# Optimization experiments

Measured on AMD Instinct MI355X. Metric: run time of the kernel, lower is better.

Reference implementation:

```python
import jax, jax.numpy as jnp
import numpy as np

N_NODES = 100000
N_EDGES = 1600000
NFEAT = 128
NHID = 128
NCLASS = 40


def setup_inputs() -> dict:
    key = jax.random.key(0)
    ks = jax.random.split(key, 12)
    s = 0.05
    return {
        "x": jax.random.normal(ks[0], (N_NODES, NFEAT), jnp.float32),
        "edge_index": jax.random.randint(ks[1], (2, N_EDGES), 0, N_NODES, jnp.int64),
        "W_pre": jax.random.normal(ks[2], (NHID, NFEAT), jnp.float32) * s,
        "b_pre": jax.random.normal(ks[3], (NHID,), jnp.float32) * s,
        "Wl0": jax.random.normal(ks[4], (NHID, NHID), jnp.float32) * s,
        "bl0": jax.random.normal(ks[5], (NHID,), jnp.float32) * s,
        "Wr0": jax.random.normal(ks[6], (NHID, NHID), jnp.float32) * s,
        "Wl1": jax.random.normal(ks[7], (NHID, NHID), jnp.float32) * s,
        "bl1": jax.random.normal(ks[8], (NHID,), jnp.float32) * s,
        "Wr1": jax.random.normal(ks[9], (NHID, NHID), jnp.float32) * s,
        "W_post": jax.random.normal(ks[10], (NCLASS, NHID), jnp.float32) * s,
        "b_post": jax.random.normal(ks[11], (NCLASS,), jnp.float32) * s,
    }


def _sage_conv(x, src, dst, Wl, bl, Wr):
    # PyG SAGEConv (mean aggr): out = lin_l(mean_{j->i} x_j) + lin_r(x_i)
    n = x.shape[0]
    agg = jax.ops.segment_sum(x[src], dst, num_segments=n)  # [N, H]
    cnt = jax.ops.segment_sum(jnp.ones((src.shape[0],), x.dtype), dst, num_segments=n)
    agg = agg / jnp.maximum(cnt, 1.0)[:, None]
    return agg @ Wl.T + bl + x @ Wr.T


def reference(x, edge_index, W_pre, b_pre, Wl0, bl0, Wr0, Wl1, bl1, Wr1, W_post, b_post):
    src, dst = edge_index[0], edge_index[1]
    h = x @ W_pre.T + b_pre  # pre-linear
    h = jax.nn.relu(_sage_conv(h, src, dst, Wl0, bl0, Wr0))  # dropout identity (eval)
    h = jax.nn.relu(_sage_conv(h, src, dst, Wl1, bl1, Wr1))
    logits = h @ W_post.T + b_post
    return jax.nn.log_softmax(logits, axis=1)
```

## Files before the change

kernel.cpp:

```cpp
#include <hip/hip_runtime.h>
#include <hip/hip_bf16.h>
#include <math.h>

#define N_NODES 100000
#define N_EDGES 1600000
#define NF 128
#define NC 40

#define NB 256
#define NPB 391
#define CAP 8192
#define PART_BLOCKS 512
#define PART_E ((N_EDGES + PART_BLOCKS - 1) / PART_BLOCKS)

#define WB_ELEMS (5 * 16384 + 48 * 128)

typedef __attribute__((ext_vector_type(8))) short short8v;
typedef __attribute__((ext_vector_type(4))) float f32x4;
typedef __attribute__((ext_vector_type(2))) float f32x2;
typedef unsigned short ushort_t;

__device__ inline float bflo(unsigned v) { union { unsigned u; float f; } x; x.u = v << 16; return x.f; }
__device__ inline float bfhi(unsigned v) { union { unsigned u; float f; } x; x.u = v & 0xffff0000u; return x.f; }
__device__ inline ushort_t f2bf(float f) {
    __hip_bfloat16 h = __float2bfloat16(f);
    return __builtin_bit_cast(ushort_t, h);
}

__device__ inline void acc_fp8x8p(uint2 v, f32x2& a0, f32x2& a1, f32x2& a2, f32x2& a3) {
    a0 += __builtin_amdgcn_cvt_pk_f32_fp8((int)v.x, false);
    a1 += __builtin_amdgcn_cvt_pk_f32_fp8((int)v.x, true);
    a2 += __builtin_amdgcn_cvt_pk_f32_fp8((int)v.y, false);
    a3 += __builtin_amdgcn_cvt_pk_f32_fp8((int)v.y, true);
}

__device__ inline short8v cvt_f32x8_bf16(float4 f0, float4 f1) {
    short8v v;
    v[0] = (short)f2bf(f0.x); v[1] = (short)f2bf(f0.y);
    v[2] = (short)f2bf(f0.z); v[3] = (short)f2bf(f0.w);
    v[4] = (short)f2bf(f1.x); v[5] = (short)f2bf(f1.y);
    v[6] = (short)f2bf(f1.z); v[7] = (short)f2bf(f1.w);
    return v;
}


__global__ __launch_bounds__(256) void k_part(const int* __restrict__ src,
                                              const int* __restrict__ dst,
                                              unsigned* __restrict__ bcur,
                                              uint2* __restrict__ pairs) {
    __shared__ unsigned cnt[NB];
    __shared__ unsigned curs[NB];
    const int t = threadIdx.x;
    cnt[t] = 0;
    __syncthreads();
    const int e0 = blockIdx.x * PART_E;
    int e1 = e0 + PART_E; if (e1 > N_EDGES) e1 = N_EDGES;
    for (int e = e0 + t; e < e1; e += 256)
        atomicAdd(&cnt[dst[e] / NPB], 1u);
    __syncthreads();
    unsigned c = cnt[t];
    curs[t] = c ? atomicAdd(&bcur[t], c) : 0u;
    __syncthreads();
    for (int e = e0 + t; e < e1; e += 256) {
        int d = dst[e];
        int s = src[e];
        int b = d / NPB;
        unsigned p = atomicAdd(&curs[b], 1u);
        if (p < CAP) pairs[(size_t)b * CAP + p] = make_uint2((unsigned)d, (unsigned)s);
    }
}

__global__ void k_bscan(const unsigned* __restrict__ bcur,
                        unsigned* __restrict__ bbase,
                        unsigned* __restrict__ rowptr) {
    __shared__ unsigned s[NB];
    const int t = threadIdx.x;
    unsigned v = bcur[t];
    s[t] = v; __syncthreads();
    for (int off = 1; off < NB; off <<= 1) {
        unsigned u = (t >= off) ? s[t - off] : 0;
        __syncthreads();
        s[t] += u;
        __syncthreads();
    }
    bbase[t] = s[t] - v;
    if (t == NB - 1) rowptr[N_NODES] = s[NB - 1];
}

__global__ __launch_bounds__(256) void k_bucket(const uint2* __restrict__ pairs,
                                                const unsigned* __restrict__ bcur,
                                                const unsigned* __restrict__ bbase,
                                                unsigned* __restrict__ rowptr,
                                                unsigned* __restrict__ srcs) {
    __shared__ unsigned s[512];
    const int t = threadIdx.x;
    const int b = blockIdx.x;
    unsigned cnt = bcur[b]; if (cnt > CAP) cnt = CAP;
    const unsigned base = bbase[b];
    const int n0 = b * NPB;
    int nn = N_NODES - n0; if (nn > NPB) nn = NPB;
    const uint2* pp = pairs + (size_t)b * CAP;

    s[t] = 0; s[t + 256] = 0;
    __syncthreads();
    for (unsigned i = t; i < cnt; i += 256)
        atomicAdd(&s[pp[i].x - n0], 1u);
    __syncthreads();
    unsigned d0 = s[t], d1 = s[t + 256];
    for (int off = 1; off < 512; off <<= 1) {
        unsigned u0 = (t >= off) ? s[t - off] : 0;
        unsigned u1 = (t + 256 >= off) ? s[t + 256 - off] : 0;
        __syncthreads();
        s[t] += u0; s[t + 256] += u1;
        __syncthreads();
    }
    unsigned ex0 = base + s[t] - d0;
    unsigned ex1 = base + s[t + 256] - d1;
    __syncthreads();
    s[t] = ex0; s[t + 256] = ex1;
    if (t < nn) rowptr[n0 + t] = ex0;
    if (t + 256 < nn) rowptr[n0 + t + 256] = ex1;
    __syncthreads();
    for (unsigned i = t; i < cnt; i += 256) {
        uint2 e = pp[i];
        unsigned p = atomicAdd(&s[e.x - n0], 1u);
        srcs[p] = e.y;
    }
}


__global__ void k_castw(const float* __restrict__ w0, const float* __restrict__ w1,
                        const float* __restrict__ w2, const float* __restrict__ w3,
                        const float* __restrict__ w4, const float* __restrict__ wp,
                        ushort_t* __restrict__ out) {
    int i = blockIdx.x * 256 + threadIdx.x;
    if (i < 5 * 16384) {
        int m = i >> 14, j = i & 16383;
        const float* s = (m == 0) ? w0 : (m == 1) ? w1 : (m == 2) ? w2 : (m == 3) ? w3 : w4;
        out[i] = f2bf(s[j]);
    } else if (i < WB_ELEMS) {
        int j = i - 5 * 16384;
        int row = j >> 7, col = j & 127;
        out[i] = (row < NC) ? f2bf(wp[row * NF + col]) : (ushort_t)0;
    }
}


__global__ __launch_bounds__(256) void k_aggregate8(const uint2* __restrict__ h64,
                                                    const unsigned* __restrict__ rowptr,
                                                    const unsigned* __restrict__ srcs,
                                                    ushort_t* __restrict__ agg) {
    int wave = threadIdx.x >> 6;
    int lane = threadIdx.x & 63;
    int node = blockIdx.x * 4 + wave;
    if (node >= N_NODES) return;
    const int slot = lane >> 4;
    const int d = lane & 15;
    unsigned beg = rowptr[node], end = rowptr[node + 1];
    f32x2 a0 = {0.f, 0.f}, a1 = {0.f, 0.f}, a2 = {0.f, 0.f}, a3 = {0.f, 0.f};
    unsigned i = beg;
    for (; i + 16 <= end; i += 16) {
        unsigned s0 = srcs[i + slot];
        unsigned s1 = srcs[i + 4 + slot];
        unsigned s2 = srcs[i + 8 + slot];
        unsigned s3 = srcs[i + 12 + slot];
        uint2 v0 = h64[(size_t)s0 * 16 + d];
        uint2 v1 = h64[(size_t)s1 * 16 + d];
        uint2 v2 = h64[(size_t)s2 * 16 + d];
        uint2 v3 = h64[(size_t)s3 * 16 + d];
        acc_fp8x8p(v0, a0, a1, a2, a3);
        acc_fp8x8p(v1, a0, a1, a2, a3);
        acc_fp8x8p(v2, a0, a1, a2, a3);
        acc_fp8x8p(v3, a0, a1, a2, a3);
    }
    if (i + 8 <= end) {
        unsigned s0 = srcs[i + slot];
        unsigned s1 = srcs[i + 4 + slot];
        uint2 v0 = h64[(size_t)s0 * 16 + d];
        uint2 v1 = h64[(size_t)s1 * 16 + d];
        acc_fp8x8p(v0, a0, a1, a2, a3);
        acc_fp8x8p(v1, a0, a1, a2, a3);
        i += 8;
    }
    if (i + 4 <= end) {
        unsigned s0 = srcs[i + slot];
        uint2 v0 = h64[(size_t)s0 * 16 + d];
        acc_fp8x8p(v0, a0, a1, a2, a3);
        i += 4;
    }
    if (i + slot < end) {
        unsigned s0 = srcs[i + slot];
        uint2 v0 = h64[(size_t)s0 * 16 + d];
        acc_fp8x8p(v0, a0, a1, a2, a3);
    }
    float r[8] = {a0.x, a0.y, a1.x, a1.y, a2.x, a2.y, a3.x, a3.y};
#pragma unroll
    for (int j = 0; j < 8; ++j) {
        r[j] += __shfl_xor(r[j], 16, 64);
        r[j] += __shfl_xor(r[j], 32, 64);
    }
    if (slot == 0) {
        float sc = 1.f / fmaxf((float)(end - beg), 1.f);
        uint4 o;
        o.x = ((unsigned)f2bf(r[1] * sc) << 16) | (unsigned)f2bf(r[0] * sc);
        o.y = ((unsigned)f2bf(r[3] * sc) << 16) | (unsigned)f2bf(r[2] * sc);
        o.z = ((unsigned)f2bf(r[5] * sc) << 16) | (unsigned)f2bf(r[4] * sc);
        o.w = ((unsigned)f2bf(r[7] * sc) << 16) | (unsigned)f2bf(r[6] * sc);
        ((uint4*)(agg + (size_t)node * NF))[d] = o;
    }
}


template <int SRC_F32, int HAS2>
__global__ __launch_bounds__(512, 4) void k_gemm2(const void* __restrict__ A1v,
                                                  const ushort_t* __restrict__ A2,
                                                  const ushort_t* __restrict__ W1,
                                                  const ushort_t* __restrict__ W2,
                                                  const float* __restrict__ bias,
                                                  ushort_t* __restrict__ out,
                                                  unsigned char* __restrict__ out8) {
    constexpr int WLDS = HAS2 ? 65536 : 32768;
    __shared__ char ldsc[WLDS + 16384];
    char* wbl = ldsc + WLDS;
    const int t = threadIdx.x;
    const int lane = t & 63;
    const int wv = t >> 6;
    const int lr = lane & 15;
    const int kg = lane >> 4;
    const int tile0 = blockIdx.x * 2;

    {
        const int n1 = 128 * 16;
        for (int c = t; c < n1; c += 512) {
            int row = c >> 4, s16 = c & 15;
            uint4 v = ((const uint4*)(W1 + (size_t)row * NF))[s16];
            *(uint4*)(&ldsc[row * 256 + ((s16 * 16) ^ ((row & 7) << 4))]) = v;
        }
        if (HAS2) {
            for (int c = t; c < n1; c += 512) {
                int row = c >> 4, s16 = c & 15;
                uint4 v = ((const uint4*)(W2 + (size_t)row * NF))[s16];
                int lrow = 128 + row;
                *(uint4*)(&ldsc[lrow * 256 + ((s16 * 16) ^ ((lrow & 7) << 4))]) = v;
            }
        }
    }

    float bv[8];
#pragma unroll
    for (int ct = 0; ct < 8; ++ct) bv[ct] = bias[ct * 16 + lr];

    auto do_mfma = [&](short8v (&a1)[4], short8v (&a2)[4], f32x4 (&ac)[8]) {
#pragma unroll
        for (int ct = 0; ct < 8; ++ct) ac[ct] = (f32x4){0.f, 0.f, 0.f, 0.f};
#pragma unroll
        for (int ct = 0; ct < 8; ++ct) {
#pragma unroll
            for (int ks = 0; ks < 4; ++ks) {
                int row = ct * 16 + lr;
                short8v b = *(const short8v*)(&ldsc[row * 256 + ((ks * 64 + kg * 16) ^ ((row & 7) << 4))]);
                ac[ct] = __builtin_amdgcn_mfma_f32_16x16x32_bf16(a1[ks], b, ac[ct], 0, 0, 0);
            }
            if (HAS2) {
#pragma unroll
                for (int ks = 0; ks < 4; ++ks) {
                    int row = 128 + ct * 16 + lr;
                    short8v b = *(const short8v*)(&ldsc[row * 256 + ((ks * 64 + kg * 16) ^ ((row & 7) << 4))]);
                    ac[ct] = __builtin_amdgcn_mfma_f32_16x16x32_bf16(a2[ks], b, ac[ct], 0, 0, 0);
                }
            }
        }
    };

    auto writeback = [&](int tile, f32x4 (&ac)[8]) {
#pragma unroll
        for (int pass = 0; pass < 2; ++pass) {
            __syncthreads();
            if ((wv >> 2) == pass) {
#pragma unroll
                for (int ct = 0; ct < 8; ++ct) {
#pragma unroll
                    for (int r = 0; r < 4; ++r) {
                        float v = ac[ct][r] + bv[ct];
                        if (!SRC_F32) v = fmaxf(v, 0.f);
                        int row = (wv & 3) * 16 + kg * 4 + r;
                        int boff = (ct * 32 + lr * 2) ^ ((row & 7) << 4);
                        *(ushort_t*)(&wbl[row * 256 + boff]) = f2bf(v);
                    }
                }
            }
            __syncthreads();
            const int u = t & 255;
            const int row = u >> 2, seg = u & 3;
            const int grow = tile * 128 + pass * 64 + row;
            uint4 vv[4];
#pragma unroll
            for (int k = 0; k < 4; ++k) {
                int s16 = seg * 4 + k;
                vv[k] = *(const uint4*)(&wbl[row * 256 + ((s16 * 16) ^ ((row & 7) << 4))]);
            }
            if (grow < N_NODES) {
                if (t < 256) {
                    uint4* op = (uint4*)(out + (size_t)grow * NF);
#pragma unroll
                    for (int k = 0; k < 4; ++k) op[seg * 4 + k] = vv[k];
                } else {
                    const unsigned* uu = (const unsigned*)vv;
                    unsigned f8[8];
#pragma unroll
                    for (int k = 0; k < 8; ++k) {
                        int p0 = __builtin_amdgcn_cvt_pk_fp8_f32(bflo(uu[2 * k]), bfhi(uu[2 * k]), 0, false);
                        f8[k] = (unsigned)__builtin_amdgcn_cvt_pk_fp8_f32(bflo(uu[2 * k + 1]), bfhi(uu[2 * k + 1]), p0, true);
                    }
                    uint4* o8 = (uint4*)(out8 + (size_t)grow * NF + seg * 32);
                    o8[0] = make_uint4(f8[0], f8[1], f8[2], f8[3]);
                    o8[1] = make_uint4(f8[4], f8[5], f8[6], f8[7]);
                }
            }
        }
    };

    short8v afA1[4], afA2[4];
    {
        int arow = tile0 * 128 + wv * 16 + lr;
        if (arow >= N_NODES) arow = N_NODES - 1;
        if (SRC_F32) {
            const float* x = (const float*)A1v;
#pragma unroll
            for (int ks = 0; ks < 4; ++ks) {
                const float4* xp = (const float4*)(x + (size_t)arow * NF + ks * 32 + kg * 8);
                afA1[ks] = cvt_f32x8_bf16(xp[0], xp[1]);
            }
        } else {
            const short8v* p = (const short8v*)((const ushort_t*)A1v + (size_t)arow * NF + kg * 8);
#pragma unroll
            for (int ks = 0; ks < 4; ++ks) afA1[ks] = p[ks * 4];
        }
        if (HAS2) {
            const short8v* p2 = (const short8v*)(A2 + (size_t)arow * NF + kg * 8);
#pragma unroll
            for (int ks = 0; ks < 4; ++ks) afA2[ks] = p2[ks * 4];
        }
    }
    __syncthreads();

    f32x4 acc[8];
    do_mfma(afA1, afA2, acc);

    short8v afB1[4], afB2[4];
    float4 rawB[8];
    {
        int arow = (tile0 + 1) * 128 + wv * 16 + lr;
        if (arow >= N_NODES) arow = N_NODES - 1;
        if (SRC_F32) {
            const float* x = (const float*)A1v;
#pragma unroll
            for (int ks = 0; ks < 4; ++ks) {
                const float4* xp = (const float4*)(x + (size_t)arow * NF + ks * 32 + kg * 8);
                rawB[2 * ks] = xp[0];
                rawB[2 * ks + 1] = xp[1];
            }
        } else {
            const short8v* p = (const short8v*)((const ushort_t*)A1v + (size_t)arow * NF + kg * 8);
#pragma unroll
            for (int ks = 0; ks < 4; ++ks) afB1[ks] = p[ks * 4];
        }
        if (HAS2) {
            const short8v* p2 = (const short8v*)(A2 + (size_t)arow * NF + kg * 8);
#pragma unroll
            for (int ks = 0; ks < 4; ++ks) afB2[ks] = p2[ks * 4];
        }
    }

    writeback(tile0, acc);

    if (SRC_F32) {
#pragma unroll
        for (int ks = 0; ks < 4; ++ks)
            afB1[ks] = cvt_f32x8_bf16(rawB[2 * ks], rawB[2 * ks + 1]);
    }

    do_mfma(afB1, afB2, acc);
    writeback(tile0 + 1, acc);
}


template <int SRC_F32, int HAS2, int POST>
__global__ __launch_bounds__(512) void k_gemm(const void* __restrict__ A1v,
                                              const ushort_t* __restrict__ A2,
                                              const ushort_t* __restrict__ W1,
                                              const ushort_t* __restrict__ W2,
                                              const float* __restrict__ bias,
                                              ushort_t* __restrict__ out,
                                              unsigned char* __restrict__ out8,
                                              const ushort_t* __restrict__ Wp,
                                              const float* __restrict__ bp,
                                              float* __restrict__ outf) {
    constexpr int LDSZ = (HAS2 ? 65536 : 32768) + (POST ? 12288 : 0);
    __shared__ char ldsc[LDSZ];
    const int t = threadIdx.x;
    const int lane = t & 63;
    const int wv = t >> 6;
    const int r0 = blockIdx.x * 128 + wv * 16;
    const int lr = lane & 15;
    const int kg = lane >> 4;

    {
        const int nchunk1 = 128 * 16;
        for (int c = t; c < nchunk1; c += 512) {
            int row = c >> 4, s16 = c & 15;
            uint4 v = ((const uint4*)(W1 + (size_t)row * NF))[s16];
            *(uint4*)(&ldsc[row * 256 + ((s16 * 16) ^ ((row & 7) << 4))]) = v;
        }
        if (HAS2) {
            for (int c = t; c < nchunk1; c += 512) {
                int row = c >> 4, s16 = c & 15;
                uint4 v = ((const uint4*)(W2 + (size_t)row * NF))[s16];
                int lrow = 128 + row;
                *(uint4*)(&ldsc[lrow * 256 + ((s16 * 16) ^ ((lrow & 7) << 4))]) = v;
            }
        }
        if (POST) {
            for (int c = t; c < 48 * 16; c += 512) {
                int row = c >> 4, s16 = c & 15;
                uint4 v = ((const uint4*)(Wp + (size_t)row * NF))[s16];
                int lrow = 256 + row;
                *(uint4*)(&ldsc[lrow * 256 + ((s16 * 16) ^ ((lrow & 7) << 4))]) = v;
            }
        }
    }

    int arow = r0 + lr;
    if (arow >= N_NODES) arow = N_NODES - 1;
    short8v af1[4], af2[4];
    if (SRC_F32) {
        const float* x = (const float*)A1v;
#pragma unroll
        for (int ks = 0; ks < 4; ++ks) {
            const float4* xp = (const float4*)(x + (size_t)arow * NF + ks * 32 + kg * 8);
            af1[ks] = cvt_f32x8_bf16(xp[0], xp[1]);
        }
    } else {
        const ushort_t* A1 = (const ushort_t*)A1v;
        const short8v* a1p = (const short8v*)(A1 + (size_t)arow * NF + kg * 8);
#pragma unroll
        for (int ks = 0; ks < 4; ++ks) af1[ks] = a1p[ks * 4];
    }
    if (HAS2) {
        const short8v* a2p = (const short8v*)(A2 + (size_t)arow * NF + kg * 8);
#pragma unroll
        for (int ks = 0; ks < 4; ++ks) af2[ks] = a2p[ks * 4];
    }
    __syncthreads();

    f32x4 acc[8];
#pragma unroll
    for (int ct = 0; ct < 8; ++ct) acc[ct] = (f32x4){0.f, 0.f, 0.f, 0.f};
#pragma unroll
    for (int ct = 0; ct < 8; ++ct) {
#pragma unroll
        for (int ks = 0; ks < 4; ++ks) {
            int row = ct * 16 + lr;
            short8v b = *(const short8v*)(&ldsc[row * 256 + ((ks * 64 + kg * 16) ^ ((row & 7) << 4))]);
            acc[ct] = __builtin_amdgcn_mfma_f32_16x16x32_bf16(af1[ks], b, acc[ct], 0, 0, 0);
        }
        if (HAS2) {
#pragma unroll
            for (int ks = 0; ks < 4; ++ks) {
                int row = 128 + ct * 16 + lr;
                short8v b = *(const short8v*)(&ldsc[row * 256 + ((ks * 64 + kg * 16) ^ ((row & 7) << 4))]);
                acc[ct] = __builtin_amdgcn_mfma_f32_16x16x32_bf16(af2[ks], b, acc[ct], 0, 0, 0);
            }
        }
    }

    {
        __syncthreads();
#pragma unroll
        for (int ct = 0; ct < 8; ++ct) {
            float bvv = bias[ct * 16 + lr];
#pragma unroll
            for (int r = 0; r < 4; ++r) {
                float v = fmaxf(acc[ct][r] + bvv, 0.f);
                int row = wv * 16 + kg * 4 + r;
                int boff = (ct * 32 + lr * 2) ^ ((row & 7) << 4);
                *(ushort_t*)(&ldsc[row * 256 + boff]) = f2bf(v);
            }
        }
        __syncthreads();

        const int lrow = wv * 16 + lr;
        short8v afp[4];
#pragma unroll
        for (int ks = 0; ks < 4; ++ks) {
            int boff = (ks * 64 + kg * 16) ^ ((lrow & 7) << 4);
            afp[ks] = *(const short8v*)(&ldsc[lrow * 256 + boff]);
        }
        f32x4 accp[3];
#pragma unroll
        for (int cp = 0; cp < 3; ++cp) accp[cp] = (f32x4){0.f, 0.f, 0.f, 0.f};
#pragma unroll
        for (int cp = 0; cp < 3; ++cp) {
#pragma unroll
            for (int ks = 0; ks < 4; ++ks) {
                int row = 256 + cp * 16 + lr;
                short8v b = *(const short8v*)(&ldsc[row * 256 + ((ks * 64 + kg * 16) ^ ((row & 7) << 4))]);
                accp[cp] = __builtin_amdgcn_mfma_f32_16x16x32_bf16(afp[ks], b, accp[cp], 0, 0, 0);
            }
        }
        float bp0 = bp[lr];
        float bp1 = bp[16 + lr];
        float bp2 = (lr < 8) ? bp[32 + lr] : 0.f;
#pragma unroll
        for (int r = 0; r < 4; ++r) {
            float v0 = accp[0][r] + bp0;
            float v1 = accp[1][r] + bp1;
            float v2 = (lr < 8) ? (accp[2][r] + bp2) : -INFINITY;
            float m = fmaxf(fmaxf(v0, v1), v2);
#pragma unroll
            for (int off = 8; off; off >>= 1) m = fmaxf(m, __shfl_xor(m, off, 16));
            float s = expf(v0 - m) + expf(v1 - m) + ((lr < 8) ? expf(v2 - m) : 0.f);
#pragma unroll
            for (int off = 8; off; off >>= 1) s += __shfl_xor(s, off, 16);
            float ls = m + logf(s);
            int node = r0 + kg * 4 + r;
            if (node < N_NODES) {
                outf[(size_t)node * NC + lr] = v0 - ls;
                outf[(size_t)node * NC + 16 + lr] = v1 - ls;
                if (lr < 8) outf[(size_t)node * NC + 32 + lr] = v2 - ls;
            }
        }
    }
}


extern "C" void kernel_launch(void* const* d_in, const int* in_sizes, int n_in,
                              void* d_out, int out_size, void* d_ws, size_t ws_size,
                              hipStream_t stream) {
    const float* x      = (const float*)d_in[0];
    const int*   ei     = (const int*)d_in[1];
    const float* W_pre  = (const float*)d_in[2];
    const float* b_pre  = (const float*)d_in[3];
    const float* Wl0    = (const float*)d_in[4];
    const float* bl0    = (const float*)d_in[5];
    const float* Wr0    = (const float*)d_in[6];
    const float* Wl1    = (const float*)d_in[7];
    const float* bl1    = (const float*)d_in[8];
    const float* Wr1    = (const float*)d_in[9];
    const float* W_post = (const float*)d_in[10];
    const float* b_post = (const float*)d_in[11];
    const int* src = ei;
    const int* dst = ei + N_EDGES;

    const size_t act_bytes = (size_t)N_NODES * NF * 2;
    const size_t act8_bytes = (size_t)N_NODES * NF;
    char* w = (char*)d_ws;
    ushort_t* h0   = (ushort_t*)w; w += act_bytes;
    ushort_t* h1   = (ushort_t*)w; w += act_bytes;
    ushort_t* aggb = (ushort_t*)w; w += act_bytes;
    unsigned char* h0f8 = (unsigned char*)w; w += act8_bytes;
    unsigned char* h1f8 = (unsigned char*)w; w += act8_bytes;
    ushort_t* wb   = (ushort_t*)w; w += (size_t)WB_ELEMS * 2;
    unsigned* rowptr = (unsigned*)w; w += (size_t)(N_NODES + 32) * 4;
    unsigned* bcur   = (unsigned*)w; w += 256 * 4;
    unsigned* bbase  = (unsigned*)w; w += 256 * 4;
    unsigned* srcs   = (unsigned*)w; w += (size_t)N_EDGES * 4;
    uint2* pairs     = (uint2*)w;   w += (size_t)NB * CAP * 8;

    ushort_t* wb_pre  = wb;
    ushort_t* wb_l0   = wb + 16384;
    ushort_t* wb_r0   = wb + 2 * 16384;
    ushort_t* wb_l1   = wb + 3 * 16384;
    ushort_t* wb_r1   = wb + 4 * 16384;
    ushort_t* wb_post = wb + 5 * 16384;

    float* outp = (float*)d_out;

    hipMemsetAsync(bcur, 0, NB * 4, stream);
    k_part<<<PART_BLOCKS, 256, 0, stream>>>(src, dst, bcur, pairs);
    k_bscan<<<1, NB, 0, stream>>>(bcur, bbase, rowptr);
    k_bucket<<<NB, 256, 0, stream>>>(pairs, bcur, bbase, rowptr, srcs);

    k_castw<<<(WB_ELEMS + 255) / 256, 256, 0, stream>>>(W_pre, Wl0, Wr0, Wl1, Wr1, W_post, wb);

    const int g2 = (N_NODES + 255) / 256;
    const int gemm_grid = (N_NODES + 127) / 128;
    const int node_grid = (N_NODES + 3) / 4;

    k_gemm2<1, 0><<<g2, 512, 0, stream>>>(x, nullptr, wb_pre, nullptr, b_pre, h0, h0f8);
    k_aggregate8<<<node_grid, 256, 0, stream>>>((const uint2*)h0f8, rowptr, srcs, aggb);
    k_gemm2<0, 1><<<g2, 512, 0, stream>>>(aggb, h0, wb_l0, wb_r0, bl0, h1, h1f8);
    k_aggregate8<<<node_grid, 256, 0, stream>>>((const uint2*)h1f8, rowptr, srcs, aggb);
    k_gemm<0, 1, 1><<<gemm_grid, 512, 0, stream>>>(aggb, h1, wb_l1, wb_r1, bl1, nullptr, nullptr,
                                                   wb_post, b_post, outp);
}
```

Before: 216.9 us.

## Merge pre-linear GEMM, edge partition and weight cast into one front kernel

Replaces the separate edge partition, weight cast and pre-linear GEMM launches with one heterogeneous kernel whose blocks are split by role, so these independent stages run concurrently and two launches disappear. The pre-linear GEMM now reads W_pre in fp32 and casts it while staging into LDS, so W_pre no longer needs a separate cast pass. The conv0 GEMM now processes four tiles per block instead of two, and the final GEMM is specialised into a dedicated post kernel. The merged kernel mixes LDS-heavy GEMM blocks with atomic-heavy partition blocks, which may affect occupancy, and conv0 uses fewer blocks.

```diff
diff --git a/kernel.cpp b/kernel.cpp
--- a/kernel.cpp
+++ b/kernel.cpp
@@ -13,7 +13,7 @@
 #define PART_BLOCKS 512
 #define PART_E ((N_EDGES + PART_BLOCKS - 1) / PART_BLOCKS)
 
-#define WB_ELEMS (5 * 16384 + 48 * 128)
+#define WB2_ELEMS (4 * 16384 + 48 * 128)
 
 typedef __attribute__((ext_vector_type(8))) short short8v;
 typedef __attribute__((ext_vector_type(4))) float f32x4;
@@ -44,31 +44,243 @@
 }
 
 
-__global__ __launch_bounds__(256) void k_part(const int* __restrict__ src,
-                                              const int* __restrict__ dst,
-                                              unsigned* __restrict__ bcur,
-                                              uint2* __restrict__ pairs) {
-    __shared__ unsigned cnt[NB];
-    __shared__ unsigned curs[NB];
+template <int SRC_F32, int HAS2, int WF32, int NT>
+__device__ __forceinline__ void gemm_body(char* ldsc, int tile0,
+                                          const void* A1v, const ushort_t* A2,
+                                          const void* W1v, const ushort_t* W2,
+                                          const float* bias,
+                                          ushort_t* out, unsigned char* out8) {
+    char* wbl = ldsc + (HAS2 ? 65536 : 32768);
     const int t = threadIdx.x;
-    cnt[t] = 0;
-    __syncthreads();
-    const int e0 = blockIdx.x * PART_E;
-    int e1 = e0 + PART_E; if (e1 > N_EDGES) e1 = N_EDGES;
-    for (int e = e0 + t; e < e1; e += 256)
-        atomicAdd(&cnt[dst[e] / NPB], 1u);
-    __syncthreads();
-    unsigned c = cnt[t];
-    curs[t] = c ? atomicAdd(&bcur[t], c) : 0u;
-    __syncthreads();
-    for (int e = e0 + t; e < e1; e += 256) {
-        int d = dst[e];
-        int s = src[e];
-        int b = d / NPB;
-        unsigned p = atomicAdd(&curs[b], 1u);
-        if (p < CAP) pairs[(size_t)b * CAP + p] = make_uint2((unsigned)d, (unsigned)s);
-    }
-}
+    const int lane = t & 63;
+    const int wv = t >> 6;
+    const int lr = lane & 15;
+    const int kg = lane >> 4;
+
+    {
+        const int n1 = 128 * 16;
+        if (WF32) {
+            const float* Wf = (const float*)W1v;
+            for (int c = t; c < n1; c += 512) {
+                int row = c >> 4, s16 = c & 15;
+                const float4* wp = (const float4*)(Wf + (size_t)row * NF) + s16 * 2;
+                short8v v = cvt_f32x8_bf16(wp[0], wp[1]);
+                *(short8v*)(&ldsc[row * 256 + ((s16 * 16) ^ ((row & 7) << 4))]) = v;
+            }
+        } else {
+            const ushort_t* W1 = (const ushort_t*)W1v;
+            for (int c = t; c < n1; c += 512) {
+                int row = c >> 4, s16 = c & 15;
+                uint4 v = ((const uint4*)(W1 + (size_t)row * NF))[s16];
+                *(uint4*)(&ldsc[row * 256 + ((s16 * 16) ^ ((row & 7) << 4))]) = v;
+            }
+        }
+        if (HAS2) {
+            for (int c = t; c < n1; c += 512) {
+                int row = c >> 4, s16 = c & 15;
+                uint4 v = ((const uint4*)(W2 + (size_t)row * NF))[s16];
+                int lrow = 128 + row;
+                *(uint4*)(&ldsc[lrow * 256 + ((s16 * 16) ^ ((lrow & 7) << 4))]) = v;
+            }
+        }
+    }
+
+    float bv[8];
+#pragma unroll
+    for (int ct = 0; ct < 8; ++ct) bv[ct] = bias[ct * 16 + lr];
+
+    auto loadA = [&](int tile, short8v (&a1)[4], short8v (&a2)[4], float4 (&raw)[8]) {
+        int arow = tile * 128 + wv * 16 + lr;
+        if (arow >= N_NODES) arow = N_NODES - 1;
+        if (SRC_F32) {
+            const float* x = (const float*)A1v;
+#pragma unroll
+            for (int ks = 0; ks < 4; ++ks) {
+                const float4* xp = (const float4*)(x + (size_t)arow * NF + ks * 32 + kg * 8);
+                raw[2 * ks] = xp[0];
+                raw[2 * ks + 1] = xp[1];
+            }
+        } else {
+            const short8v* p = (const short8v*)((const ushort_t*)A1v + (size_t)arow * NF + kg * 8);
+#pragma unroll
+            for (int ks = 0; ks < 4; ++ks) a1[ks] = p[ks * 4];
+        }
+        if (HAS2) {
+            const short8v* p2 = (const short8v*)(A2 + (size_t)arow * NF + kg * 8);
+#pragma unroll
+            for (int ks = 0; ks < 4; ++ks) a2[ks] = p2[ks * 4];
+        }
+    };
+
+    auto do_mfma = [&](short8v (&a1)[4], short8v (&a2)[4], f32x4 (&ac)[8]) {
+#pragma unroll
+        for (int ct = 0; ct < 8; ++ct) ac[ct] = (f32x4){0.f, 0.f, 0.f, 0.f};
+#pragma unroll
+        for (int ct = 0; ct < 8; ++ct) {
+#pragma unroll
+            for (int ks = 0; ks < 4; ++ks) {
+                int row = ct * 16 + lr;
+                short8v b = *(const short8v*)(&ldsc[row * 256 + ((ks * 64 + kg * 16) ^ ((row & 7) << 4))]);
+                ac[ct] = __builtin_amdgcn_mfma_f32_16x16x32_bf16(a1[ks], b, ac[ct], 0, 0, 0);
+            }
+            if (HAS2) {
+#pragma unroll
+                for (int ks = 0; ks < 4; ++ks) {
+                    int row = 128 + ct * 16 + lr;
+                    short8v b = *(const short8v*)(&ldsc[row * 256 + ((ks * 64 + kg * 16) ^ ((row & 7) << 4))]);
+                    ac[ct] = __builtin_amdgcn_mfma_f32_16x16x32_bf16(a2[ks], b, ac[ct], 0, 0, 0);
+                }
+            }
+        }
+    };
+
+    auto writeback = [&](int tile, f32x4 (&ac)[8]) {
+#pragma unroll
+        for (int pass = 0; pass < 2; ++pass) {
+            __syncthreads();
+            if ((wv >> 2) == pass) {
+#pragma unroll
+                for (int ct = 0; ct < 8; ++ct) {
+#pragma unroll
+                    for (int r = 0; r < 4; ++r) {
+                        float v = ac[ct][r] + bv[ct];
+                        if (!SRC_F32) v = fmaxf(v, 0.f);
+                        int row = (wv & 3) * 16 + kg * 4 + r;
+                        int boff = (ct * 32 + lr * 2) ^ ((row & 7) << 4);
+                        *(ushort_t*)(&wbl[row * 256 + boff]) = f2bf(v);
+                    }
+                }
+            }
+            __syncthreads();
+            const int u = t & 255;
+            const int row = u >> 2, seg = u & 3;
+            const int grow = tile * 128 + pass * 64 + row;
+            uint4 vv[4];
+#pragma unroll
+            for (int k = 0; k < 4; ++k) {
+                int s16 = seg * 4 + k;
+                vv[k] = *(const uint4*)(&wbl[row * 256 + ((s16 * 16) ^ ((row & 7) << 4))]);
+            }
+            if (grow < N_NODES) {
+                if (t < 256) {
+                    uint4* op = (uint4*)(out + (size_t)grow * NF);
+#pragma unroll
+                    for (int k = 0; k < 4; ++k) op[seg * 4 + k] = vv[k];
+                } else {
+                    const unsigned* uu = (const unsigned*)vv;
+                    unsigned f8[8];
+#pragma unroll
+                    for (int k = 0; k < 8; ++k) {
+                        int p0 = __builtin_amdgcn_cvt_pk_fp8_f32(bflo(uu[2 * k]), bfhi(uu[2 * k]), 0, false);
+                        f8[k] = (unsigned)__builtin_amdgcn_cvt_pk_fp8_f32(bflo(uu[2 * k + 1]), bfhi(uu[2 * k + 1]), p0, true);
+                    }
+                    uint4* o8 = (uint4*)(out8 + (size_t)grow * NF + seg * 32);
+                    o8[0] = make_uint4(f8[0], f8[1], f8[2], f8[3]);
+                    o8[1] = make_uint4(f8[4], f8[5], f8[6], f8[7]);
+                }
+            }
+        }
+    };
+
+    short8v aC1[4], aC2[4], aN1[4], aN2[4];
+    float4 rawC[8], rawN[8];
+    loadA(tile0, aC1, aC2, rawC);
+    __syncthreads();
+    if (SRC_F32) {
+#pragma unroll
+        for (int ks = 0; ks < 4; ++ks) aC1[ks] = cvt_f32x8_bf16(rawC[2 * ks], rawC[2 * ks + 1]);
+    }
+
+    f32x4 acc[8];
+#pragma unroll
+    for (int j = 0; j < NT; ++j) {
+        do_mfma(aC1, aC2, acc);
+        if (j + 1 < NT) loadA(tile0 + j + 1, aN1, aN2, rawN);
+        writeback(tile0 + j, acc);
+        if (j + 1 < NT) {
+            if (SRC_F32) {
+#pragma unroll
+                for (int ks = 0; ks < 4; ++ks) aN1[ks] = cvt_f32x8_bf16(rawN[2 * ks], rawN[2 * ks + 1]);
+            }
+#pragma unroll
+            for (int ks = 0; ks < 4; ++ks) {
+                aC1[ks] = aN1[ks];
+                if (HAS2) aC2[ks] = aN2[ks];
+            }
+        }
+    }
+}
+
+
+__global__ __launch_bounds__(512, 4) void k_front(const float* __restrict__ x,
+                                                  const float* __restrict__ W_pre,
+                                                  const float* __restrict__ b_pre,
+                                                  ushort_t* __restrict__ h0,
+                                                  unsigned char* __restrict__ h0f8,
+                                                  const int* __restrict__ src,
+                                                  const int* __restrict__ dst,
+                                                  unsigned* __restrict__ bcur,
+                                                  uint2* __restrict__ pairs,
+                                                  const float* __restrict__ wl0,
+                                                  const float* __restrict__ wr0,
+                                                  const float* __restrict__ wl1,
+                                                  const float* __restrict__ wr1,
+                                                  const float* __restrict__ wpost,
+                                                  ushort_t* __restrict__ wbout) {
+    __shared__ char ldsc[49152];
+    const int bid = blockIdx.x;
+    const int t = threadIdx.x;
+    if (bid < 391) {
+        gemm_body<1, 0, 1, 2>(ldsc, bid * 2, x, nullptr, W_pre, nullptr, b_pre, h0, h0f8);
+    } else if (bid < 903) {
+        unsigned* cnt = (unsigned*)ldsc;
+        unsigned* curs = cnt + NB;
+        if (t < NB) cnt[t] = 0;
+        __syncthreads();
+        const int e0 = (bid - 391) * PART_E;
+        int e1 = e0 + PART_E; if (e1 > N_EDGES) e1 = N_EDGES;
+        for (int e = e0 + t; e < e1; e += 512)
+            atomicAdd(&cnt[dst[e] / NPB], 1u);
+        __syncthreads();
+        if (t < NB) {
+            unsigned c = cnt[t];
+            curs[t] = c ? atomicAdd(&bcur[t], c) : 0u;
+        }
+        __syncthreads();
+        for (int e = e0 + t; e < e1; e += 512) {
+            int d = dst[e];
+            int s = src[e];
+            int b = d / NPB;
+            unsigned p = atomicAdd(&curs[b], 1u);
+            if (p < CAP) pairs[(size_t)b * CAP + p] = make_uint2((unsigned)d, (unsigned)s);
+        }
+    } else {
+        for (int i = t; i < WB2_ELEMS; i += 512) {
+            if (i < 4 * 16384) {
+                int m = i >> 14, j = i & 16383;
+                const float* s = (m == 0) ? wl0 : (m == 1) ? wr0 : (m == 2) ? wl1 : wr1;
+                wbout[i] = f2bf(s[j]);
+            } else {
+                int j = i - 4 * 16384;
+                int row = j >> 7, col = j & 127;
+                wbout[i] = (row < NC) ? f2bf(wpost[row * NF + col]) : (ushort_t)0;
+            }
+        }
+    }
+}
+
+
+__global__ __launch_bounds__(512, 4) void k_conv0(const ushort_t* __restrict__ A1,
+                                                  const ushort_t* __restrict__ A2,
+                                                  const ushort_t* __restrict__ W1,
+                                                  const ushort_t* __restrict__ W2,
+                                                  const float* __restrict__ bias,
+                                                  ushort_t* __restrict__ out,
+                                                  unsigned char* __restrict__ out8) {
+    __shared__ char ldsc[81920];
+    gemm_body<0, 1, 0, 4>(ldsc, blockIdx.x * 4, A1, A2, W1, W2, bias, out, out8);
+}
+
 
 __global__ void k_bscan(const unsigned* __restrict__ bcur,
                         unsigned* __restrict__ bbase,
@@ -125,23 +337,6 @@
         uint2 e = pp[i];
         unsigned p = atomicAdd(&s[e.x - n0], 1u);
         srcs[p] = e.y;
-    }
-}
-
-
-__global__ void k_castw(const float* __restrict__ w0, const float* __restrict__ w1,
-                        const float* __restrict__ w2, const float* __restrict__ w3,
-                        const float* __restrict__ w4, const float* __restrict__ wp,
-                        ushort_t* __restrict__ out) {
-    int i = blockIdx.x * 256 + threadIdx.x;
-    if (i < 5 * 16384) {
-        int m = i >> 14, j = i & 16383;
-        const float* s = (m == 0) ? w0 : (m == 1) ? w1 : (m == 2) ? w2 : (m == 3) ? w3 : w4;
-        out[i] = f2bf(s[j]);
-    } else if (i < WB_ELEMS) {
-        int j = i - 5 * 16384;
-        int row = j >> 7, col = j & 127;
-        out[i] = (row < NC) ? f2bf(wp[row * NF + col]) : (ushort_t)0;
     }
 }
 
@@ -211,193 +406,15 @@
 }
 
 
-template <int SRC_F32, int HAS2>
-__global__ __launch_bounds__(512, 4) void k_gemm2(const void* __restrict__ A1v,
-                                                  const ushort_t* __restrict__ A2,
-                                                  const ushort_t* __restrict__ W1,
-                                                  const ushort_t* __restrict__ W2,
-                                                  const float* __restrict__ bias,
-                                                  ushort_t* __restrict__ out,
-                                                  unsigned char* __restrict__ out8) {
-    constexpr int WLDS = HAS2 ? 65536 : 32768;
-    __shared__ char ldsc[WLDS + 16384];
-    char* wbl = ldsc + WLDS;
-    const int t = threadIdx.x;
-    const int lane = t & 63;
-    const int wv = t >> 6;
-    const int lr = lane & 15;
-    const int kg = lane >> 4;
-    const int tile0 = blockIdx.x * 2;
-
-    {
-        const int n1 = 128 * 16;
-        for (int c = t; c < n1; c += 512) {
-            int row = c >> 4, s16 = c & 15;
-            uint4 v = ((const uint4*)(W1 + (size_t)row * NF))[s16];
-            *(uint4*)(&ldsc[row * 256 + ((s16 * 16) ^ ((row & 7) << 4))]) = v;
-        }
-        if (HAS2) {
-            for (int c = t; c < n1; c += 512) {
-                int row = c >> 4, s16 = c & 15;
-                uint4 v = ((const uint4*)(W2 + (size_t)row * NF))[s16];
-                int lrow = 128 + row;
-                *(uint4*)(&ldsc[lrow * 256 + ((s16 * 16) ^ ((lrow & 7) << 4))]) = v;
-            }
-        }
-    }
-
-    float bv[8];
-#pragma unroll
-    for (int ct = 0; ct < 8; ++ct) bv[ct] = bias[ct * 16 + lr];
-
-    auto do_mfma = [&](short8v (&a1)[4], short8v (&a2)[4], f32x4 (&ac)[8]) {
-#pragma unroll
-        for (int ct = 0; ct < 8; ++ct) ac[ct] = (f32x4){0.f, 0.f, 0.f, 0.f};
-#pragma unroll
-        for (int ct = 0; ct < 8; ++ct) {
-#pragma unroll
-            for (int ks = 0; ks < 4; ++ks) {
-                int row = ct * 16 + lr;
-                short8v b = *(const short8v*)(&ldsc[row * 256 + ((ks * 64 + kg * 16) ^ ((row & 7) << 4))]);
-                ac[ct] = __builtin_amdgcn_mfma_f32_16x16x32_bf16(a1[ks], b, ac[ct], 0, 0, 0);
-            }
-            if (HAS2) {
-#pragma unroll
-                for (int ks = 0; ks < 4; ++ks) {
-                    int row = 128 + ct * 16 + lr;
-                    short8v b = *(const short8v*)(&ldsc[row * 256 + ((ks * 64 + kg * 16) ^ ((row & 7) << 4))]);
-                    ac[ct] = __builtin_amdgcn_mfma_f32_16x16x32_bf16(a2[ks], b, ac[ct], 0, 0, 0);
-                }
-            }
-        }
-    };
-
-    auto writeback = [&](int tile, f32x4 (&ac)[8]) {
-#pragma unroll
-        for (int pass = 0; pass < 2; ++pass) {
-            __syncthreads();
-            if ((wv >> 2) == pass) {
-#pragma unroll
-                for (int ct = 0; ct < 8; ++ct) {
-#pragma unroll
-                    for (int r = 0; r < 4; ++r) {
-                        float v = ac[ct][r] + bv[ct];
-                        if (!SRC_F32) v = fmaxf(v, 0.f);
-                        int row = (wv & 3) * 16 + kg * 4 + r;
-                        int boff = (ct * 32 + lr * 2) ^ ((row & 7) << 4);
-                        *(ushort_t*)(&wbl[row * 256 + boff]) = f2bf(v);
-                    }
-                }
-            }
-            __syncthreads();
-            const int u = t & 255;
-            const int row = u >> 2, seg = u & 3;
-            const int grow = tile * 128 + pass * 64 + row;
-            uint4 vv[4];
-#pragma unroll
-            for (int k = 0; k < 4; ++k) {
-                int s16 = seg * 4 + k;
-                vv[k] = *(const uint4*)(&wbl[row * 256 + ((s16 * 16) ^ ((row & 7) << 4))]);
-            }
-            if (grow < N_NODES) {
-                if (t < 256) {
-                    uint4* op = (uint4*)(out + (size_t)grow * NF);
-#pragma unroll
-                    for (int k = 0; k < 4; ++k) op[seg * 4 + k] = vv[k];
-                } else {
-                    const unsigned* uu = (const unsigned*)vv;
-                    unsigned f8[8];
-#pragma unroll
-                    for (int k = 0; k < 8; ++k) {
-                        int p0 = __builtin_amdgcn_cvt_pk_fp8_f32(bflo(uu[2 * k]), bfhi(uu[2 * k]), 0, false);
-                        f8[k] = (unsigned)__builtin_amdgcn_cvt_pk_fp8_f32(bflo(uu[2 * k + 1]), bfhi(uu[2 * k + 1]), p0, true);
-                    }
-                    uint4* o8 = (uint4*)(out8 + (size_t)grow * NF + seg * 32);
-                    o8[0] = make_uint4(f8[0], f8[1], f8[2], f8[3]);
-                    o8[1] = make_uint4(f8[4], f8[5], f8[6], f8[7]);
-                }
-            }
-        }
-    };
-
-    short8v afA1[4], afA2[4];
-    {
-        int arow = tile0 * 128 + wv * 16 + lr;
-        if (arow >= N_NODES) arow = N_NODES - 1;
-        if (SRC_F32) {
-            const float* x = (const float*)A1v;
-#pragma unroll
-            for (int ks = 0; ks < 4; ++ks) {
-                const float4* xp = (const float4*)(x + (size_t)arow * NF + ks * 32 + kg * 8);
-                afA1[ks] = cvt_f32x8_bf16(xp[0], xp[1]);
-            }
-        } else {
-            const short8v* p = (const short8v*)((const ushort_t*)A1v + (size_t)arow * NF + kg * 8);
-#pragma unroll
-            for (int ks = 0; ks < 4; ++ks) afA1[ks] = p[ks * 4];
-        }
-        if (HAS2) {
-            const short8v* p2 = (const short8v*)(A2 + (size_t)arow * NF + kg * 8);
-#pragma unroll
-            for (int ks = 0; ks < 4; ++ks) afA2[ks] = p2[ks * 4];
-        }
-    }
-    __syncthreads();
-
-    f32x4 acc[8];
-    do_mfma(afA1, afA2, acc);
-
-    short8v afB1[4], afB2[4];
-    float4 rawB[8];
-    {
-        int arow = (tile0 + 1) * 128 + wv * 16 + lr;
-        if (arow >= N_NODES) arow = N_NODES - 1;
-        if (SRC_F32) {
-            const float* x = (const float*)A1v;
-#pragma unroll
-            for (int ks = 0; ks < 4; ++ks) {
-                const float4* xp = (const float4*)(x + (size_t)arow * NF + ks * 32 + kg * 8);
-                rawB[2 * ks] = xp[0];
-                rawB[2 * ks + 1] = xp[1];
-            }
-        } else {
-            const short8v* p = (const short8v*)((const ushort_t*)A1v + (size_t)arow * NF + kg * 8);
-#pragma unroll
-            for (int ks = 0; ks < 4; ++ks) afB1[ks] = p[ks * 4];
-        }
-        if (HAS2) {
-            const short8v* p2 = (const short8v*)(A2 + (size_t)arow * NF + kg * 8);
-#pragma unroll
-            for (int ks = 0; ks < 4; ++ks) afB2[ks] = p2[ks * 4];
-        }
-    }
-
-    writeback(tile0, acc);
-
-    if (SRC_F32) {
-#pragma unroll
-        for (int ks = 0; ks < 4; ++ks)
-            afB1[ks] = cvt_f32x8_bf16(rawB[2 * ks], rawB[2 * ks + 1]);
-    }
-
-    do_mfma(afB1, afB2, acc);
-    writeback(tile0 + 1, acc);
-}
-
-
-template <int SRC_F32, int HAS2, int POST>
-__global__ __launch_bounds__(512) void k_gemm(const void* __restrict__ A1v,
-                                              const ushort_t* __restrict__ A2,
-                                              const ushort_t* __restrict__ W1,
-                                              const ushort_t* __restrict__ W2,
-                                              const float* __restrict__ bias,
-                                              ushort_t* __restrict__ out,
-                                              unsigned char* __restrict__ out8,
-                                              const ushort_t* __restrict__ Wp,
-                                              const float* __restrict__ bp,
-                                              float* __restrict__ outf) {
-    constexpr int LDSZ = (HAS2 ? 65536 : 32768) + (POST ? 12288 : 0);
-    __shared__ char ldsc[LDSZ];
+__global__ __launch_bounds__(512) void k_gemm_post(const ushort_t* __restrict__ A1,
+                                                   const ushort_t* __restrict__ A2,
+                                                   const ushort_t* __restrict__ W1,
+                                                   const ushort_t* __restrict__ W2,
+                                                   const float* __restrict__ bias,
+                                                   const ushort_t* __restrict__ Wp,
+                                                   const float* __restrict__ bp,
+                                                   float* __restrict__ outf) {
+    __shared__ char ldsc[65536 + 12288];
     const int t = threadIdx.x;
     const int lane = t & 63;
     const int wv = t >> 6;
@@ -412,41 +429,27 @@
             uint4 v = ((const uint4*)(W1 + (size_t)row * NF))[s16];
             *(uint4*)(&ldsc[row * 256 + ((s16 * 16) ^ ((row & 7) << 4))]) = v;
         }
-        if (HAS2) {
-            for (int c = t; c < nchunk1; c += 512) {
-                int row = c >> 4, s16 = c & 15;
-                uint4 v = ((const uint4*)(W2 + (size_t)row * NF))[s16];
-                int lrow = 128 + row;
-                *(uint4*)(&ldsc[lrow * 256 + ((s16 * 16) ^ ((lrow & 7) << 4))]) = v;
-            }
-        }
-        if (POST) {
-            for (int c = t; c < 48 * 16; c += 512) {
-                int row = c >> 4, s16 = c & 15;
-                uint4 v = ((const uint4*)(Wp + (size_t)row * NF))[s16];
-                int lrow = 256 + row;
-                *(uint4*)(&ldsc[lrow * 256 + ((s16 * 16) ^ ((lrow & 7) << 4))]) = v;
-            }
+        for (int c = t; c < nchunk1; c += 512) {
+            int row = c >> 4, s16 = c & 15;
+            uint4 v = ((const uint4*)(W2 + (size_t)row * NF))[s16];
+            int lrow = 128 + row;
+            *(uint4*)(&ldsc[lrow * 256 + ((s16 * 16) ^ ((lrow & 7) << 4))]) = v;
+        }
+        for (int c = t; c < 48 * 16; c += 512) {
+            int row = c >> 4, s16 = c & 15;
+            uint4 v = ((const uint4*)(Wp + (size_t)row * NF))[s16];
+            int lrow = 256 + row;
+            *(uint4*)(&ldsc[lrow * 256 + ((s16 * 16) ^ ((lrow & 7) << 4))]) = v;
         }
     }
 
     int arow = r0 + lr;
     if (arow >= N_NODES) arow = N_NODES - 1;
     short8v af1[4], af2[4];
-    if (SRC_F32) {
-        const float* x = (const float*)A1v;
-#pragma unroll
-        for (int ks = 0; ks < 4; ++ks) {
-            const float4* xp = (const float4*)(x + (size_t)arow * NF + ks * 32 + kg * 8);
-            af1[ks] = cvt_f32x8_bf16(xp[0], xp[1]);
-        }
-    } else {
-        const ushort_t* A1 = (const ushort_t*)A1v;
+    {
         const short8v* a1p = (const short8v*)(A1 + (size_t)arow * NF + kg * 8);
 #pragma unroll
         for (int ks = 0; ks < 4; ++ks) af1[ks] = a1p[ks * 4];
-    }
-    if (HAS2) {
         const short8v* a2p = (const short8v*)(A2 + (size_t)arow * NF + kg * 8);
 #pragma unroll
         for (int ks = 0; ks < 4; ++ks) af2[ks] = a2p[ks * 4];
@@ -464,71 +467,67 @@
             short8v b = *(const short8v*)(&ldsc[row * 256 + ((ks * 64 + kg * 16) ^ ((row & 7) << 4))]);
             acc[ct] = __builtin_amdgcn_mfma_f32_16x16x32_bf16(af1[ks], b, acc[ct], 0, 0, 0);
         }
-        if (HAS2) {
-#pragma unroll
-            for (int ks = 0; ks < 4; ++ks) {
-                int row = 128 + ct * 16 + lr;
-                short8v b = *(const short8v*)(&ldsc[row * 256 + ((ks * 64 + kg * 16) ^ ((row & 7) << 4))]);
-                acc[ct] = __builtin_amdgcn_mfma_f32_16x16x32_bf16(af2[ks], b, acc[ct], 0, 0, 0);
-            }
-        }
-    }
-
-    {
-        __syncthreads();
-#pragma unroll
-        for (int ct = 0; ct < 8; ++ct) {
-            float bvv = bias[ct * 16 + lr];
-#pragma unroll
-            for (int r = 0; r < 4; ++r) {
-                float v = fmaxf(acc[ct][r] + bvv, 0.f);
-                int row = wv * 16 + kg * 4 + r;
-                int boff = (ct * 32 + lr * 2) ^ ((row & 7) << 4);
-                *(ushort_t*)(&ldsc[row * 256 + boff]) = f2bf(v);
-            }
-        }
-        __syncthreads();
-
-        const int lrow = wv * 16 + lr;
-        short8v afp[4];
 #pragma unroll
         for (int ks = 0; ks < 4; ++ks) {
-            int boff = (ks * 64 + kg * 16) ^ ((lrow & 7) << 4);
-            afp[ks] = *(const short8v*)(&ldsc[lrow * 256 + boff]);
-        }
-        f32x4 accp[3];
-#pragma unroll
-        for (int cp = 0; cp < 3; ++cp) accp[cp] = (f32x4){0.f, 0.f, 0.f, 0.f};
-#pragma unroll
-        for (int cp = 0; cp < 3; ++cp) {
-#pragma unroll
-            for (int ks = 0; ks < 4; ++ks) {
-                int row = 256 + cp * 16 + lr;
-                short8v b = *(const short8v*)(&ldsc[row * 256 + ((ks * 64 + kg * 16) ^ ((row & 7) << 4))]);
-                accp[cp] = __builtin_amdgcn_mfma_f32_16x16x32_bf16(afp[ks], b, accp[cp], 0, 0, 0);
-            }
-        }
-        float bp0 = bp[lr];
-        float bp1 = bp[16 + lr];
-        float bp2 = (lr < 8) ? bp[32 + lr] : 0.f;
+            int row = 128 + ct * 16 + lr;
+            short8v b = *(const short8v*)(&ldsc[row * 256 + ((ks * 64 + kg * 16) ^ ((row & 7) << 4))]);
+            acc[ct] = __builtin_amdgcn_mfma_f32_16x16x32_bf16(af2[ks], b, acc[ct], 0, 0, 0);
+        }
+    }
+
+    __syncthreads();
+#pragma unroll
+    for (int ct = 0; ct < 8; ++ct) {
+        float bvv = bias[ct * 16 + lr];
 #pragma unroll
         for (int r = 0; r < 4; ++r) {
-            float v0 = accp[0][r] + bp0;
-            float v1 = accp[1][r] + bp1;
-            float v2 = (lr < 8) ? (accp[2][r] + bp2) : -INFINITY;
-            float m = fmaxf(fmaxf(v0, v1), v2);
-#pragma unroll
-            for (int off = 8; off; off >>= 1) m = fmaxf(m, __shfl_xor(m, off, 16));
-            float s = expf(v0 - m) + expf(v1 - m) + ((lr < 8) ? expf(v2 - m) : 0.f);
-#pragma unroll
-            for (int off = 8; off; off >>= 1) s += __shfl_xor(s, off, 16);
-            float ls = m + logf(s);
-            int node = r0 + kg * 4 + r;
-            if (node < N_NODES) {
-                outf[(size_t)node * NC + lr] = v0 - ls;
-                outf[(size_t)node * NC + 16 + lr] = v1 - ls;
-                if (lr < 8) outf[(size_t)node * NC + 32 + lr] = v2 - ls;
-            }
+            float v = fmaxf(acc[ct][r] + bvv, 0.f);
+            int row = wv * 16 + kg * 4 + r;
+            int boff = (ct * 32 + lr * 2) ^ ((row & 7) << 4);
+            *(ushort_t*)(&ldsc[row * 256 + boff]) = f2bf(v);
+        }
+    }
+    __syncthreads();
+
+    const int lrow = wv * 16 + lr;
+    short8v afp[4];
+#pragma unroll
+    for (int ks = 0; ks < 4; ++ks) {
+        int boff = (ks * 64 + kg * 16) ^ ((lrow & 7) << 4);
+        afp[ks] = *(const short8v*)(&ldsc[lrow * 256 + boff]);
+    }
+    f32x4 accp[3];
+#pragma unroll
+    for (int cp = 0; cp < 3; ++cp) accp[cp] = (f32x4){0.f, 0.f, 0.f, 0.f};
+#pragma unroll
+    for (int cp = 0; cp < 3; ++cp) {
+#pragma unroll
+        for (int ks = 0; ks < 4; ++ks) {
+            int row = 256 + cp * 16 + lr;
+            short8v b = *(const short8v*)(&ldsc[row * 256 + ((ks * 64 + kg * 16) ^ ((row & 7) << 4))]);
+            accp[cp] = __builtin_amdgcn_mfma_f32_16x16x32_bf16(afp[ks], b, accp[cp], 0, 0, 0);
+        }
+    }
+    float bp0 = bp[lr];
+    float bp1 = bp[16 + lr];
+    float bp2 = (lr < 8) ? bp[32 + lr] : 0.f;
+#pragma unroll
+    for (int r = 0; r < 4; ++r) {
+        float v0 = accp[0][r] + bp0;
+        float v1 = accp[1][r] + bp1;
+        float v2 = (lr < 8) ? (accp[2][r] + bp2) : -INFINITY;
+        float m = fmaxf(fmaxf(v0, v1), v2);
+#pragma unroll
+        for (int off = 8; off; off >>= 1) m = fmaxf(m, __shfl_xor(m, off, 16));
+        float s = expf(v0 - m) + expf(v1 - m) + ((lr < 8) ? expf(v2 - m) : 0.f);
+#pragma unroll
+        for (int off = 8; off; off >>= 1) s += __shfl_xor(s, off, 16);
+        float ls = m + logf(s);
+        int node = r0 + kg * 4 + r;
+        if (node < N_NODES) {
+            outf[(size_t)node * NC + lr] = v0 - ls;
+            outf[(size_t)node * NC + 16 + lr] = v1 - ls;
+            if (lr < 8) outf[(size_t)node * NC + 32 + lr] = v2 - ls;
         }
     }
 }
@@ -560,37 +559,33 @@
     ushort_t* aggb = (ushort_t*)w; w += act_bytes;
     unsigned char* h0f8 = (unsigned char*)w; w += act8_bytes;
     unsigned char* h1f8 = (unsigned char*)w; w += act8_bytes;
-    ushort_t* wb   = (ushort_t*)w; w += (size_t)WB_ELEMS * 2;
+    ushort_t* wb   = (ushort_t*)w; w += (size_t)WB2_ELEMS * 2;
     unsigned* rowptr = (unsigned*)w; w += (size_t)(N_NODES + 32) * 4;
     unsigned* bcur   = (unsigned*)w; w += 256 * 4;
     unsigned* bbase  = (unsigned*)w; w += 256 * 4;
     unsigned* srcs   = (unsigned*)w; w += (size_t)N_EDGES * 4;
     uint2* pairs     = (uint2*)w;   w += (size_t)NB * CAP * 8;
 
-    ushort_t* wb_pre  = wb;
-    ushort_t* wb_l0   = wb + 16384;
-    ushort_t* wb_r0   = wb + 2 * 16384;
-    ushort_t* wb_l1   = wb + 3 * 16384;
-    ushort_t* wb_r1   = wb + 4 * 16384;
-    ushort_t* wb_post = wb + 5 * 16384;
+    ushort_t* wb_l0   = wb;
+    ushort_t* wb_r0   = wb + 16384;
+    ushort_t* wb_l1   = wb + 2 * 16384;
+    ushort_t* wb_r1   = wb + 3 * 16384;
+    ushort_t* wb_post = wb + 4 * 16384;
 
     float* outp = (float*)d_out;
 
+    const int node_grid = (N_NODES + 3) / 4;
+    const int conv1_grid = (N_NODES + 127) / 128;
+    const int conv0_grid = (conv1_grid + 3) / 4;
+
     hipMemsetAsync(bcur, 0, NB * 4, stream);
-    k_part<<<PART_BLOCKS, 256, 0, stream>>>(src, dst, bcur, pairs);
+    k_front<<<904, 512, 0, stream>>>(x, W_pre, b_pre, h0, h0f8, src, dst, bcur, pairs,
+                                     Wl0, Wr0, Wl1, Wr1, W_post, wb);
     k_bscan<<<1, NB, 0, stream>>>(bcur, bbase, rowptr);
     k_bucket<<<NB, 256, 0, stream>>>(pairs, bcur, bbase, rowptr, srcs);
-
-    k_castw<<<(WB_ELEMS + 255) / 256, 256, 0, stream>>>(W_pre, Wl0, Wr0, Wl1, Wr1, W_post, wb);
-
-    const int g2 = (N_NODES + 255) / 256;
-    const int gemm_grid = (N_NODES + 127) / 128;
-    const int node_grid = (N_NODES + 3) / 4;
-
-    k_gemm2<1, 0><<<g2, 512, 0, stream>>>(x, nullptr, wb_pre, nullptr, b_pre, h0, h0f8);
     k_aggregate8<<<node_grid, 256, 0, stream>>>((const uint2*)h0f8, rowptr, srcs, aggb);
-    k_gemm2<0, 1><<<g2, 512, 0, stream>>>(aggb, h0, wb_l0, wb_r0, bl0, h1, h1f8);
+    k_conv0<<<conv0_grid, 512, 0, stream>>>(aggb, h0, wb_l0, wb_r0, bl0, h1, h1f8);
     k_aggregate8<<<node_grid, 256, 0, stream>>>((const uint2*)h1f8, rowptr, srcs, aggb);
-    k_gemm<0, 1, 1><<<gemm_grid, 512, 0, stream>>>(aggb, h1, wb_l1, wb_r1, bl1, nullptr, nullptr,
-                                                   wb_post, b_post, outp);
-}
+    k_gemm_post<<<conv1_grid, 512, 0, stream>>>(aggb, h1, wb_l1, wb_r1, bl1,
+                                                wb_post, b_post, outp);
+}
```

Result: slower. 295.8 us (+36.4%).
